# Optimization experiments

Measured on AMD Instinct MI355X. Metric: run time of the kernel, lower is better.

Reference implementation:

```python
import jax, jax.numpy as jnp
import numpy as np

NI, ND, NH = 64, 64, 4
NB, NLOC, NNEI = 4, 2048, 64


def setup_inputs() -> dict:
    key = jax.random.key(0)
    ks = jax.random.split(key, 7)
    g1 = jax.random.normal(ks[0], (NB, NLOC, NI), dtype=jnp.float32)
    gg1 = jax.random.normal(ks[1], (NB, NLOC, NNEI, NI), dtype=jnp.float32)
    nlist_mask = jax.random.randint(ks[2], (NB, NLOC, NNEI), 0, 2).astype(bool)
    # torch Linear weight (out, in); store transposed for x @ W
    Wq = jax.random.normal(ks[3], (NI, ND * NH), dtype=jnp.float32) * (1.0 / np.sqrt(NI))
    Wkv = jax.random.normal(ks[4], (NI, (ND + NI) * NH), dtype=jnp.float32) * (1.0 / np.sqrt(NI))
    Wh = jax.random.normal(ks[5], (NI * NH, NI), dtype=jnp.float32) * (1.0 / np.sqrt(NI * NH))
    bh = jax.random.normal(ks[6], (NI,), dtype=jnp.float32) * 0.01
    return {"g1": g1, "gg1": gg1, "nlist_mask": nlist_mask,
            "Wq": Wq, "Wkv": Wkv, "Wh": Wh, "bh": bh}


def reference(g1, gg1, nlist_mask, Wq, Wkv, Wh, bh):
    nb, nloc, nnei = nlist_mask.shape
    ni, nd, nh = NI, ND, NH
    # q: (nb, nloc, nh, nd)
    q = (g1 @ Wq).reshape(nb, nloc, nd, nh).transpose(0, 1, 3, 2)
    # kv: (nb, nloc, nnei, nd, 2*nh) -> (nb, nloc, 2*nh, nnei, nd); valid since ni == nd
    kv = (gg1 @ Wkv).reshape(nb, nloc, nnei, nd, 2 * nh).transpose(0, 1, 4, 2, 3)
    k = kv[:, :, :nh]          # (nb, nloc, nh, nnei, nd)
    v = kv[:, :, nh:2 * nh]    # (nb, nloc, nh, nnei, nd)
    attnw = jnp.einsum('blhd,blhjd->blhj', q, k) / np.sqrt(nd).astype(np.float32)
    m = nlist_mask[:, :, None, :]  # (nb, nloc, 1, nnei)
    attnw = jnp.where(m, attnw, -jnp.inf)
    attnw = jax.nn.softmax(attnw, axis=-1)
    attnw = jnp.where(m, attnw, 0.0)
    ret = jnp.einsum('blhj,blhjd->blhd', attnw, v).reshape(nb, nloc, nh * ni)
    return ret @ Wh + bh
```

## Files before the change

### kernel.cpp

```cpp
#include <hip/hip_runtime.h>
#include <hip/hip_fp16.h>
#include <math.h>

#define NATOM 8192

namespace {

typedef _Float16 half8 __attribute__((ext_vector_type(8)));
typedef float f32x4 __attribute__((ext_vector_type(4)));

constexpr int VB_STRIDE = 260;

__global__ void pack_wkv(const float* __restrict__ Wkv, _Float16* __restrict__ out) {
  int tid = blockIdx.x * 256 + threadIdx.x;
  int jj = tid & 7;
  int l  = (tid >> 3) & 63;
  int ks = (tid >> 9) & 1;
  int ct = tid >> 10;
  int i  = ks * 32 + ((l >> 4) << 3) + jj;
  int c  = ct * 16 + (l & 15);
  out[tid] = (_Float16)Wkv[i * 512 + c];
}

__global__ __launch_bounds__(256, 4)
void local_atten_kernel(const float* __restrict__ g1,
                        const float* __restrict__ gg1,
                        const int* __restrict__ mask,
                        const float* __restrict__ Wq,
                        const _Float16* __restrict__ wkvp,
                        const float* __restrict__ Wh,
                        const float* __restrict__ bh,
                        float* __restrict__ out) {
  __shared__ __align__(16) __half vraw[64 * VB_STRIDE];
  __shared__ float g1s[64];
  __shared__ __align__(16) float qs[256];
  __shared__ __half sred[4][4][64];
  __shared__ float aws[4][64];
  __shared__ __half rets[256];
  __shared__ float redbuf[4][64];

  const int t = threadIdx.x;
  const int lane = t & 63;
  const int wave = t >> 6;
  const int lq = lane >> 4;
  const int lr = lane & 15;
  const int atom = blockIdx.x;

  __half* gs = vraw;
  auto vbuf = reinterpret_cast<__half(*)[VB_STRIDE]>(vraw);

  if (t < 64) g1s[t] = g1[(size_t)atom * 64 + t];

  {
    const float4* src = reinterpret_cast<const float4*>(gg1 + (size_t)atom * 4096);
#pragma unroll
    for (int r = 0; r < 4; ++r) {
      int idx4 = t + 256 * r;
      int j = idx4 >> 4;
      int i4 = (idx4 & 15) << 2;
      float4 v = src[idx4];
      __half2 h01 = __floats2half2_rn(v.x, v.y);
      __half2 h23 = __floats2half2_rn(v.z, v.w);
      int g = i4 >> 3;
      int addr = j * 64 + ((g ^ (j & 7)) << 3) + (i4 & 7);
      union { __half2 h[2]; uint2 u; } pk;
      pk.h[0] = h01; pk.h[1] = h23;
      *reinterpret_cast<uint2*>(&gs[addr]) = pk.u;
    }
  }
  __syncthreads();

  half8 bfrag[4][2];
#pragma unroll
  for (int jt = 0; jt < 4; ++jt) {
#pragma unroll
    for (int ks = 0; ks < 2; ++ks) {
      int j = jt * 16 + lr;
      int g = ks * 4 + lq;
      bfrag[jt][ks] =
          *reinterpret_cast<const half8*>(&gs[j * 64 + ((g ^ (j & 7)) << 3)]);
    }
  }

  {
    float qacc = 0.f;
#pragma unroll 8
    for (int i = 0; i < 64; ++i) qacc = fmaf(g1s[i], Wq[i * 256 + t], qacc);
    qs[t] = qacc;
  }
  __syncthreads();

  float sacc[4][4];
#pragma unroll
  for (int jt = 0; jt < 4; ++jt)
#pragma unroll
    for (int h = 0; h < 4; ++h) sacc[jt][h] = 0.f;

  const bool isv = (lq & 1);
#pragma unroll 2
  for (int it = 0; it < 8; ++it) {
    const int ct = ((it >> 2) << 4) + wave * 4 + (it & 3);
    const half8* ap = reinterpret_cast<const half8*>(wkvp) + ct * 128;
    half8 a0 = ap[lane];
    half8 a1 = ap[64 + lane];
    const int d = ct * 2 + (lq >> 1);

    f32x4 accs[4];
#pragma unroll
    for (int jt = 0; jt < 4; ++jt) {
      f32x4 acc = {0.f, 0.f, 0.f, 0.f};
      acc = __builtin_amdgcn_mfma_f32_16x16x32_f16(a0, bfrag[jt][0], acc, 0, 0, 0);
      acc = __builtin_amdgcn_mfma_f32_16x16x32_f16(a1, bfrag[jt][1], acc, 0, 0, 0);
      accs[jt] = acc;
    }

    if (isv) {
#pragma unroll
      for (int jt = 0; jt < 4; ++jt) {
        int j = jt * 16 + lr;
        __half2 h01 = __floats2half2_rn(accs[jt][0], accs[jt][1]);
        __half2 h23 = __floats2half2_rn(accs[jt][2], accs[jt][3]);
        union { __half2 h[2]; uint2 u; } pk;
        pk.h[0] = h01; pk.h[1] = h23;
        *reinterpret_cast<uint2*>(&vbuf[j][d * 4]) = pk.u;
      }
    } else {
      float4 q4 = *reinterpret_cast<const float4*>(&qs[d * 4]);
#pragma unroll
      for (int jt = 0; jt < 4; ++jt) {
        sacc[jt][0] = fmaf(accs[jt][0], q4.x, sacc[jt][0]);
        sacc[jt][1] = fmaf(accs[jt][1], q4.y, sacc[jt][1]);
        sacc[jt][2] = fmaf(accs[jt][2], q4.z, sacc[jt][2]);
        sacc[jt][3] = fmaf(accs[jt][3], q4.w, sacc[jt][3]);
      }
    }
  }

#pragma unroll
  for (int jt = 0; jt < 4; ++jt)
#pragma unroll
    for (int h = 0; h < 4; ++h)
      sacc[jt][h] += __shfl_xor(sacc[jt][h], 32);
  if (lq == 0) {
#pragma unroll
    for (int h = 0; h < 4; ++h)
#pragma unroll
      for (int jt = 0; jt < 4; ++jt)
        sred[wave][h][jt * 16 + lr] = __float2half(sacc[jt][h]);
  }
  __syncthreads();

  {
    float s = __half2float(sred[0][wave][lane]) + __half2float(sred[1][wave][lane]) +
              __half2float(sred[2][wave][lane]) + __half2float(sred[3][wave][lane]);
    s *= 0.125f;
    const int m = mask[(size_t)atom * 64 + lane];
    s = m ? s : -INFINITY;
    float mx = s;
#pragma unroll
    for (int off = 32; off > 0; off >>= 1) mx = fmaxf(mx, __shfl_xor(mx, off));
    float pe = m ? __expf(s - mx) : 0.f;
    float sum = pe;
#pragma unroll
    for (int off = 32; off > 0; off >>= 1) sum += __shfl_xor(sum, off);
    aws[wave][lane] = (sum > 0.f) ? (pe / sum) : 0.f;
  }
  __syncthreads();

  {
    float o = 0.f;
#pragma unroll 8
    for (int j = 0; j < 64; ++j) {
      float a = aws[wave][j];
      float vv = __half2float(vbuf[j][lane * 4 + wave]);
      o = fmaf(a, vv, o);
    }
    rets[wave * 64 + lane] = __float2half(o);
  }
  __syncthreads();

  {
    float part = 0.f;
#pragma unroll 8
    for (int k = 0; k < 64; ++k)
      part = fmaf(__half2float(rets[wave * 64 + k]), Wh[(wave * 64 + k) * 64 + lane],
                  part);
    redbuf[wave][lane] = part;
  }
  __syncthreads();
  if (t < 64)
    out[(size_t)atom * 64 + t] =
        redbuf[0][t] + redbuf[1][t] + redbuf[2][t] + redbuf[3][t] + bh[t];
}

}

extern "C" void kernel_launch(void* const* d_in, const int* in_sizes, int n_in,
                              void* d_out, int out_size, void* d_ws, size_t ws_size,
                              hipStream_t stream) {
  const float* g1   = (const float*)d_in[0];
  const float* gg1  = (const float*)d_in[1];
  const int*   mask = (const int*)d_in[2];
  const float* Wq   = (const float*)d_in[3];
  const float* Wkv  = (const float*)d_in[4];
  const float* Wh   = (const float*)d_in[5];
  const float* bh   = (const float*)d_in[6];
  float* out = (float*)d_out;
  (void)in_sizes; (void)n_in; (void)ws_size; (void)out_size;

  _Float16* wkvp = (_Float16*)d_ws;
  pack_wkv<<<128, 256, 0, stream>>>(Wkv, wkvp);
  local_atten_kernel<<<NATOM, 256, 0, stream>>>(g1, gg1, mask, Wq, wkvp, Wh, bh, out);
}
```

Measured before the change: 276.4 us.

## Pre-pack Wq/Wh to fp16 and use packed dot2/hfma2 for small GEMVs

```diff
diff --git a/kernel.cpp b/kernel.cpp
--- a/kernel.cpp
+++ b/kernel.cpp
@@ -7,37 +7,64 @@
 namespace {
 
 typedef _Float16 half8 __attribute__((ext_vector_type(8)));
+typedef _Float16 half2t __attribute__((ext_vector_type(2)));
 typedef float f32x4 __attribute__((ext_vector_type(4)));
 
 constexpr int VB_STRIDE = 260;
 
-__global__ void pack_wkv(const float* __restrict__ Wkv, _Float16* __restrict__ out) {
+__global__ void pack_weights(const float* __restrict__ Wkv,
+                             const float* __restrict__ Wq,
+                             const float* __restrict__ Wh,
+                             _Float16* __restrict__ out) {
   int tid = blockIdx.x * 256 + threadIdx.x;
-  int jj = tid & 7;
-  int l  = (tid >> 3) & 63;
-  int ks = (tid >> 9) & 1;
-  int ct = tid >> 10;
-  int i  = ks * 32 + ((l >> 4) << 3) + jj;
-  int c  = ct * 16 + (l & 15);
-  out[tid] = (_Float16)Wkv[i * 512 + c];
+  if (tid < 32768) {
+    int jj = tid & 7;
+    int l  = (tid >> 3) & 63;
+    int ks = (tid >> 9) & 1;
+    int ct = tid >> 10;
+    int i  = ks * 32 + ((l >> 4) << 3) + jj;
+    int c  = ct * 16 + (l & 15);
+    out[tid] = (_Float16)Wkv[i * 512 + c];
+  } else if (tid < 49152) {
+    int idx = tid - 32768;
+    int c = idx >> 6, i = idx & 63;
+    out[tid] = (_Float16)Wq[i * 256 + c];
+  } else {
+    int idx = tid - 49152;
+    int c = idx >> 8, k = idx & 255;
+    out[tid] = (_Float16)Wh[k * 64 + c];
+  }
+}
+
+__device__ __forceinline__ float dot8(half8 a, half8 b, float acc) {
+  acc = __builtin_amdgcn_fdot2((half2t){a[0], a[1]}, (half2t){b[0], b[1]}, acc, false);
+  acc = __builtin_amdgcn_fdot2((half2t){a[2], a[3]}, (half2t){b[2], b[3]}, acc, false);
+  acc = __builtin_amdgcn_fdot2((half2t){a[4], a[5]}, (half2t){b[4], b[5]}, acc, false);
+  acc = __builtin_amdgcn_fdot2((half2t){a[6], a[7]}, (half2t){b[6], b[7]}, acc, false);
+  return acc;
 }
 
 __global__ __launch_bounds__(256, 4)
 void local_atten_kernel(const float* __restrict__ g1,
                         const float* __restrict__ gg1,
                         const int* __restrict__ mask,
-                        const float* __restrict__ Wq,
-                        const _Float16* __restrict__ wkvp,
-                        const float* __restrict__ Wh,
+                        const _Float16* __restrict__ wpack,
                         const float* __restrict__ bh,
                         float* __restrict__ out) {
   __shared__ __align__(16) __half vraw[64 * VB_STRIDE];
-  __shared__ float g1s[64];
-  __shared__ __align__(16) float qs[256];
-  __shared__ __half sred[4][4][64];
-  __shared__ float aws[4][64];
-  __shared__ __half rets[256];
-  __shared__ float redbuf[4][64];
+  __shared__ __align__(16) __half g1h[64];
+  __shared__ __align__(16) unsigned char blob[3072];
+  __shared__ __align__(8) __half aws2[64][4];
+  __shared__ __align__(16) __half rets[256];
+
+  float* qs = reinterpret_cast<float*>(blob);
+  __half (*sred)[4][64] = reinterpret_cast<__half(*)[4][64]>(blob + 1024);
+  __half (*redbuf2)[64][4] = reinterpret_cast<__half(*)[64][4]>(blob);
+  float (*redbuf)[64] = reinterpret_cast<float(*)[64]>(blob + 2048);
+
+  const _Float16* wkvp = wpack;
+  const _Float16* wqp  = wpack + 32768;
+  const _Float16* whp  = wpack + 49152;
 
   const int t = threadIdx.x;
   const int lane = t & 63;
@@ -49,7 +76,7 @@
   __half* gs = vraw;
   auto vbuf = reinterpret_cast<__half(*)[VB_STRIDE]>(vraw);
 
-  if (t < 64) g1s[t] = g1[(size_t)atom * 64 + t];
+  if (t < 64) g1h[t] = __float2half(g1[(size_t)atom * 64 + t]);
 
   {
     const float4* src = reinterpret_cast<const float4*>(gg1 + (size_t)atom * 4096);
@@ -84,8 +111,10 @@
 
   {
     float qacc = 0.f;
-#pragma unroll 8
-    for (int i = 0; i < 64; ++i) qacc = fmaf(g1s[i], Wq[i * 256 + t], qacc);
+    const half8* wrow = reinterpret_cast<const half8*>(wqp + t * 64);
+    const half8* grow = reinterpret_cast<const half8*>(&g1h[0]);
+#pragma unroll
+    for (int ks = 0; ks < 8; ++ks) qacc = dot8(wrow[ks], grow[ks], qacc);
     qs[t] = qacc;
   }
   __syncthreads();
@@ -163,28 +192,42 @@
     float sum = pe;
 #pragma unroll
     for (int off = 32; off > 0; off >>= 1) sum += __shfl_xor(sum, off);
-    aws[wave][lane] = (sum > 0.f) ? (pe / sum) : 0.f;
-  }
-  __syncthreads();
-
-  {
-    float o = 0.f;
-#pragma unroll 8
-    for (int j = 0; j < 64; ++j) {
-      float a = aws[wave][j];
-      float vv = __half2float(vbuf[j][lane * 4 + wave]);
-      o = fmaf(a, vv, o);
-    }
-    rets[wave * 64 + lane] = __float2half(o);
+    float aw = (sum > 0.f) ? (pe / sum) : 0.f;
+    aws2[lane][wave] = __float2half(aw);
+  }
+  __syncthreads();
+
+  {
+    __half2 o01 = __float2half2_rn(0.f), o23 = __float2half2_rn(0.f);
+#pragma unroll
+    for (int jj = 0; jj < 16; ++jj) {
+      int j = wave * 16 + jj;
+      union { uint2 u; __half2 h[2]; } aw, vv;
+      aw.u = *reinterpret_cast<const uint2*>(&aws2[j][0]);
+      vv.u = *reinterpret_cast<const uint2*>(&vbuf[j][lane * 4]);
+      o01 = __hfma2(aw.h[0], vv.h[0], o01);
+      o23 = __hfma2(aw.h[1], vv.h[1], o23);
+    }
+    union { uint2 u; __half2 h[2]; } pk;
+    pk.h[0] = o01; pk.h[1] = o23;
+    *reinterpret_cast<uint2*>(&redbuf2[wave][lane][0]) = pk.u;
+  }
+  __syncthreads();
+
+  {
+    float r = 0.f;
+#pragma unroll
+    for (int jq = 0; jq < 4; ++jq) r += __half2float(redbuf2[jq][lane][wave]);
+    rets[wave * 64 + lane] = __float2half(r);
   }
   __syncthreads();
 
   {
     float part = 0.f;
-#pragma unroll 8
-    for (int k = 0; k < 64; ++k)
-      part = fmaf(__half2float(rets[wave * 64 + k]), Wh[(wave * 64 + k) * 64 + lane],
-                  part);
+    const half8* wrow = reinterpret_cast<const half8*>(whp + lane * 256 + wave * 64);
+    const half8* rrow = reinterpret_cast<const half8*>(&rets[wave * 64]);
+#pragma unroll
+    for (int ks = 0; ks < 8; ++ks) part = dot8(wrow[ks], rrow[ks], part);
     redbuf[wave][lane] = part;
   }
   __syncthreads();
@@ -208,7 +251,7 @@
   float* out = (float*)d_out;
   (void)in_sizes; (void)n_in; (void)ws_size; (void)out_size;
 
-  _Float16* wkvp = (_Float16*)d_ws;
-  pack_wkv<<<128, 256, 0, stream>>>(Wkv, wkvp);
-  local_atten_kernel<<<NATOM, 256, 0, stream>>>(g1, gg1, mask, Wq, wkvp, Wh, bh, out);
-}
+  _Float16* wpack = (_Float16*)d_ws;
+  pack_weights<<<256, 256, 0, stream>>>(Wkv, Wq, Wh, wpack);
+  local_atten_kernel<<<NATOM, 256, 0, stream>>>(g1, gg1, mask, wpack, bh, out);
+}
```

Result: no change. 281.6 us (+1.9%).
